# Kernel tuning notes

Measured on AMD Instinct MI355X. Metric: run time of the kernel, lower is better.

The kernel has to match this reference:

```python
import jax, jax.numpy as jnp
import numpy as np

B, T, D_IN = 4, 4096, 1024
H, DK, DV, D_MODEL = 16, 64, 64, 1024
EPS = 1e-6


def setup_inputs() -> dict:
    key = jax.random.key(0)
    ks = jax.random.split(key, 11)
    s_in = 1.0 / np.sqrt(D_IN)
    s_o = 1.0 / np.sqrt(H * DV)
    return {
        "query": jax.random.normal(ks[0], (B, T, D_IN), jnp.float32),
        "key": jax.random.normal(ks[1], (B, T, D_IN), jnp.float32),
        "value": jax.random.normal(ks[2], (B, T, D_IN), jnp.float32),
        "Wq": jax.random.normal(ks[3], (D_IN, H * DK), jnp.float32) * s_in,
        "bq": jnp.zeros((H * DK,), jnp.float32),
        "Wk": jax.random.normal(ks[4], (D_IN, H * DK), jnp.float32) * s_in,
        "bk": jnp.zeros((H * DK,), jnp.float32),
        "Wv": jax.random.normal(ks[5], (D_IN, H * DV), jnp.float32) * s_in,
        "bv": jnp.zeros((H * DV,), jnp.float32),
        "Wo": jax.random.normal(ks[6], (H * DV, D_MODEL), jnp.float32) * s_o,
        "bo": jnp.zeros((D_MODEL,), jnp.float32),
    }


def _phi(x):
    # ELU(x) + 1 feature map (positive kernel feature)
    return jax.nn.elu(x) + 1.0


def reference(query, key, value, Wq, bq, Wk, bk, Wv, bv, Wo, bo):
    b, t, _ = query.shape
    q = _phi(query @ Wq + bq).reshape(b, t, H, DK)   # [B,T,H,DK]
    k = _phi(key @ Wk + bk).reshape(b, t, H, DK)     # [B,T,H,DK]
    v = (value @ Wv + bv).reshape(b, t, H, DV)       # [B,T,H,DV]
    # KV accumulation over time: [B,H,DV,DK]
    kv = jnp.einsum('bthd,bthk->bhkd', k, v)
    # normalizer: q . sum_t(k)  -> [B,T,H]
    norm = 1.0 / (jnp.einsum('bthd,bhd->bth', q, k.sum(axis=1)) + EPS)
    attn = jnp.einsum('bthd,bhkd,bth->bthk', q, kv, norm)  # [B,T,H,DV]
    attn = attn.reshape(b, t, H * DV)
    return attn @ Wo + bo
```

## Files before the change

### kernel.cpp

```cpp
#include <hip/hip_runtime.h>

typedef __bf16 bf16;
typedef bf16 bf16x2 __attribute__((ext_vector_type(2)));
typedef bf16 bf16x8 __attribute__((ext_vector_type(8)));
typedef float f32x4 __attribute__((ext_vector_type(4)));

#define B_ 4
#define T_ 4096
#define H_ 16
#define DK_ 64
#define DV_ 64
#define DMODEL_ 1024
#define M_ (B_ * T_)
#define EPS_ 1e-6f

#define BARX()  asm volatile("s_barrier" ::: "memory")
#define LGKM0() asm volatile("s_waitcnt lgkmcnt(0)" ::: "memory")

__device__ __forceinline__ void async_ld16(const void* g, void* l) {
    __builtin_amdgcn_global_load_lds(
        (const __attribute__((address_space(1))) unsigned int*)g,
        (__attribute__((address_space(3))) unsigned int*)l,
        16, 0, 0);
}

struct TPtrs { const float* s[4]; bf16* d[4]; };

__global__ void transpose4(TPtrs p) {
    __shared__ bf16 t[32][33];
    const float* src = p.s[blockIdx.z];
    bf16*        dst = p.d[blockIdx.z];
    const int tx = threadIdx.x, ty = threadIdx.y;
    const int x  = blockIdx.x * 32 + tx;
    const int y0 = blockIdx.y * 32 + ty;
#pragma unroll
    for (int i = 0; i < 32; i += 8)
        t[ty + i][tx] = (bf16)src[(size_t)(y0 + i) * 1024 + x];
    __syncthreads();
    const int xo = blockIdx.y * 32 + tx;
    const int yo = blockIdx.x * 32 + ty;
#pragma unroll
    for (int i = 0; i < 32; i += 8)
        dst[(size_t)(yo + i) * 1024 + xo] = t[tx][ty + i];
}

__global__ __launch_bounds__(256) void cvt_kernel(
    const float* __restrict__ src, bf16* __restrict__ dst)
{
    const size_t i = (size_t)blockIdx.x * 256 + threadIdx.x;
    const float4* s = (const float4*)src + 2 * i;
    float4 a = s[0];
    float4 b = s[1];
    bf16x8 h;
    h[0] = (bf16)a.x; h[1] = (bf16)a.y; h[2] = (bf16)a.z; h[3] = (bf16)a.w;
    h[4] = (bf16)b.x; h[5] = (bf16)b.y; h[6] = (bf16)b.z; h[7] = (bf16)b.w;
    *(bf16x8*)(dst + 8 * i) = h;
}


__device__ __forceinline__ void stage_half(
    const bf16* __restrict__ G, int base_rc, int K,
    char* lds_op_buf, int t, int h, int w, int lane)
{
    const int r8   = lane >> 3;
    const int row  = h * 128 + w * 8 + r8;
    const int cole = (((lane & 7) ^ r8) << 3);
    const bf16* g = G + (size_t)(base_rc + row) * K + t * 64 + cole;
    char* l = lds_op_buf + h * 16384 + w * 1024;
    async_ld16(g, l);
    async_ld16(g + (size_t)64 * K, l + 8192);
}

template<int G>
__device__ __forceinline__ void read_a4(bf16x8 (&aF)[4][2], const char* ab,
                                        int arow, int fq, int l7) {
#pragma unroll
    for (int i = 0; i < 4; ++i)
#pragma unroll
        for (int ks = 0; ks < 2; ++ks)
            aF[i][ks] = *(const bf16x8*)(ab
                + (arow + (G * 4 + i) * 16) * 128
                + ((((ks << 2) + fq) ^ l7) << 4));
}

template<int JP>
__device__ __forceinline__ void read_b2(bf16x8 (&bF)[4][2], const char* bb,
                                        int brow, int fq, int l7) {
#pragma unroll
    for (int j = 0; j < 2; ++j)
#pragma unroll
        for (int ks = 0; ks < 2; ++ks)
            bF[JP * 2 + j][ks] = *(const bf16x8*)(bb
                + (brow + (JP * 2 + j) * 16) * 128
                + ((((ks << 2) + fq) ^ l7) << 4));
}

template<int G, int JP>
__device__ __forceinline__ void mfma_q(f32x4 (&acc)[8][4],
                                       const bf16x8 (&aF)[4][2],
                                       const bf16x8 (&bF)[4][2]) {
#pragma unroll
    for (int i = 0; i < 4; ++i)
#pragma unroll
        for (int j = 0; j < 2; ++j)
#pragma unroll
            for (int ks = 0; ks < 2; ++ks)
                acc[G * 4 + i][JP * 2 + j] =
                    __builtin_amdgcn_mfma_f32_16x16x32_bf16(
                        aF[i][ks], bF[JP * 2 + j][ks],
                        acc[G * 4 + i][JP * 2 + j], 0, 0, 0);
}

template<int ACT, int OUTMODE>
__global__ __launch_bounds__(512, 2) void gemm256_kernel(
    const bf16* __restrict__ A, const bf16* __restrict__ Bt,
    const float* __restrict__ bias, void* __restrict__ Cout,
    int M, int N, int K)
{
    __shared__ f32x4 smem4[8192];
    char* smem = (char*)smem4;
    char* Ab0 = smem;
    char* Ab1 = smem + 32768;
    char* Bb0 = smem + 65536;
    char* Bb1 = smem + 98304;

    const int tid  = threadIdx.x;
    const int w    = tid >> 6, lane = tid & 63;
    const int wrow = w >> 2,  wcol = w & 3;
    const int fr = lane & 15, fq = lane >> 4, l7 = lane & 7;
    const int arow = wrow * 128 + fr;
    const int brow = wcol * 64 + fr;

    const int nwg  = gridDim.x * gridDim.y;
    const int flat = blockIdx.y * gridDim.x + blockIdx.x;
    const int swz  = (flat & 7) * (nwg >> 3) + (flat >> 3);
    const int n0   = (swz % gridDim.x) * 256;
    const int m0   = (swz / gridDim.x) * 256;

    const int KT = K >> 6;

    f32x4  acc[8][4] = {};
    bf16x8 aF[4][2], bF[4][2];

    stage_half(Bt, n0, K, Bb0, 0, 0, w, lane);
    stage_half(Bt, n0, K, Bb0, 0, 1, w, lane);
    stage_half(A,  m0, K, Ab0, 0, 0, w, lane);
    stage_half(A,  m0, K, Ab0, 0, 1, w, lane);
    stage_half(Bt, n0, K, Bb1, 1, 0, w, lane);
    stage_half(Bt, n0, K, Bb1, 1, 1, w, lane);
    stage_half(A,  m0, K, Ab1, 1, 0, w, lane);
    stage_half(A,  m0, K, Ab1, 1, 1, w, lane);
    asm volatile("s_waitcnt vmcnt(8)" ::: "memory");
    BARX();

    for (int it = 0; it < (KT >> 1); ++it) {
        const int  t0   = it * 2, t1 = t0 + 1;
        const bool more = (it < (KT >> 1) - 1);

        read_a4<0>(aF, Ab0, arow, fq, l7);
        read_b2<0>(bF, Bb0, brow, fq, l7);
        asm volatile("s_waitcnt lgkmcnt(8)" ::: "memory");
        BARX(); LGKM0();
        __builtin_amdgcn_s_setprio(1);
        mfma_q<0, 0>(acc, aF, bF);
        __builtin_amdgcn_s_setprio(0);
        BARX();

        read_b2<1>(bF, Bb0, brow, fq, l7);
        BARX(); LGKM0();
        __builtin_amdgcn_s_setprio(1);
        mfma_q<0, 1>(acc, aF, bF);
        __builtin_amdgcn_s_setprio(0);
        BARX();

        read_a4<1>(aF, Ab0, arow, fq, l7);
        if (more) {
            stage_half(Bt, n0, K, Bb0, t0 + 2, 0, w, lane);
            stage_half(Bt, n0, K, Bb0, t0 + 2, 1, w, lane);
        }
        BARX(); LGKM0();
        __builtin_amdgcn_s_setprio(1);
        mfma_q<1, 0>(acc, aF, bF);
        __builtin_amdgcn_s_setprio(0);
        BARX();

        if (more) {
            stage_half(A, m0, K, Ab0, t0 + 2, 0, w, lane);
            stage_half(A, m0, K, Ab0, t0 + 2, 1, w, lane);
            asm volatile("s_waitcnt vmcnt(8)" ::: "memory");
        } else {
            asm volatile("s_waitcnt vmcnt(0)" ::: "memory");
        }
        BARX();
        __builtin_amdgcn_s_setprio(1);
        mfma_q<1, 1>(acc, aF, bF);
        __builtin_amdgcn_s_setprio(0);
        BARX();

        read_a4<0>(aF, Ab1, arow, fq, l7);
        read_b2<0>(bF, Bb1, brow, fq, l7);
        asm volatile("s_waitcnt lgkmcnt(8)" ::: "memory");
        BARX(); LGKM0();
        __builtin_amdgcn_s_setprio(1);
        mfma_q<0, 0>(acc, aF, bF);
        __builtin_amdgcn_s_setprio(0);
        BARX();

        read_b2<1>(bF, Bb1, brow, fq, l7);
        BARX(); LGKM0();
        __builtin_amdgcn_s_setprio(1);
        mfma_q<0, 1>(acc, aF, bF);
        __builtin_amdgcn_s_setprio(0);
        BARX();

        read_a4<1>(aF, Ab1, arow, fq, l7);
        if (more) {
            stage_half(Bt, n0, K, Bb1, t1 + 2, 0, w, lane);
            stage_half(Bt, n0, K, Bb1, t1 + 2, 1, w, lane);
        }
        BARX(); LGKM0();
        __builtin_amdgcn_s_setprio(1);
        mfma_q<1, 0>(acc, aF, bF);
        __builtin_amdgcn_s_setprio(0);
        BARX();

        if (more) {
            stage_half(A, m0, K, Ab1, t1 + 2, 0, w, lane);
            stage_half(A, m0, K, Ab1, t1 + 2, 1, w, lane);
            asm volatile("s_waitcnt vmcnt(8)" ::: "memory");
        }
        BARX();
        __builtin_amdgcn_s_setprio(1);
        mfma_q<1, 1>(acc, aF, bF);
        __builtin_amdgcn_s_setprio(0);
        BARX();
    }

    const size_t Ns = (size_t)N;
    if constexpr (OUTMODE == 2) {
        __syncthreads();
        char* eb = smem;
#pragma unroll
        for (int g = 0; g < 8; ++g)
#pragma unroll
            for (int j = 0; j < 4; ++j) {
                const int col = wcol * 64 + j * 16 + fr;
                const float bb = bias[n0 + col];
#pragma unroll
                for (int r = 0; r < 4; ++r) {
                    float x = acc[g][j][r] + bb;
                    if (ACT) x = (x > 0.0f) ? (x + 1.0f) : __expf(x);
                    const int row = wrow * 128 + g * 16 + fq * 4 + r;
                    *(bf16*)(eb + row * 512
                        + ((((col >> 3) ^ (row & 7)) << 4) | ((col & 7) << 1)))
                        = (bf16)x;
                }
            }
        __syncthreads();
        bf16* Cp = (bf16*)Cout;
#pragma unroll
        for (int o = 0; o < 16; ++o) {
            const int n = (tid >> 3) + (o & 3) * 64;
            const int m = (tid & 7) * 8 + (o >> 2) * 64;
            bf16x8 v;
#pragma unroll
            for (int e = 0; e < 8; ++e) {
                const int row = m + e;
                v[e] = *(const bf16*)(eb + row * 512
                        + ((((n >> 3) ^ (row & 7)) << 4) | ((n & 7) << 1)));
            }
            *(bf16x8*)(Cp + (size_t)(n0 + n) * M + m0 + m) = v;
        }
    } else {
#pragma unroll
        for (int g = 0; g < 8; ++g) {
#pragma unroll
            for (int j = 0; j < 4; ++j) {
                const int col = n0 + wcol * 64 + j * 16 + fr;
                const float bb = bias[col];
                const int row0 = m0 + wrow * 128 + g * 16 + fq * 4;
#pragma unroll
                for (int r = 0; r < 4; ++r) {
                    float x = acc[g][j][r] + bb;
                    if (ACT) x = (x > 0.0f) ? (x + 1.0f) : __expf(x);
                    if (OUTMODE == 1)
                        ((float*)Cout)[(size_t)(row0 + r) * Ns + col] = x;
                    else
                        ((bf16*)Cout)[(size_t)(row0 + r) * Ns + col] = (bf16)x;
                }
            }
        }
    }
}

__global__ __launch_bounds__(256) void kv_partial_kernel(
    const bf16* __restrict__ KT, const bf16* __restrict__ VT,
    float* __restrict__ kv_part, float* __restrict__ ksum_part)
{
    const int bh = blockIdx.y, b = bh >> 4, h = bh & 15;
    const int tc = blockIdx.x;
    __shared__ char lds[32768];

    const int tid = threadIdx.x, wv = tid >> 6, lane = tid & 63;
    const int fr = lane & 15, fq = lane >> 4, l7 = lane & 7;

    const int r1 = wv * 8 + (lane >> 3);
    const int c1 = ((lane & 7) ^ (r1 & 7)) << 3;
    const size_t g1 = (size_t)(h * 64 + r1) * M_ + (size_t)b * T_ + c1;
    const size_t g2 = g1 + (size_t)32 * M_;
    const int dstoff = (wv * 64 + lane) * 16;

    f32x4 acc[4] = {};
    float ksa = 0.0f;
    const int rk = tid >> 2, qk = tid & 3;

    {
        const size_t mo = (size_t)tc * 512;
        async_ld16(VT + g1 + mo, lds + dstoff);
        async_ld16(VT + g2 + mo, lds + 4096 + dstoff);
        async_ld16(KT + g1 + mo, lds + 8192 + dstoff);
        async_ld16(KT + g2 + mo, lds + 12288 + dstoff);
    }
    for (int it = 0; it < 8; ++it) {
        char* cur = lds + (it & 1) * 16384;
        char* nxt = lds + ((it & 1) ^ 1) * 16384;
        if (it < 7) {
            const size_t mo = (size_t)tc * 512 + (it + 1) * 64;
            async_ld16(VT + g1 + mo, nxt + dstoff);
            async_ld16(VT + g2 + mo, nxt + 4096 + dstoff);
            async_ld16(KT + g1 + mo, nxt + 8192 + dstoff);
            async_ld16(KT + g2 + mo, nxt + 12288 + dstoff);
            asm volatile("s_waitcnt vmcnt(4)" ::: "memory");
        } else {
            asm volatile("s_waitcnt vmcnt(0)" ::: "memory");
        }
        BARX();
        const char* Vb = cur;
        const char* Kb = cur + 8192;
#pragma unroll
        for (int ks = 0; ks < 2; ++ks) {
            bf16x8 av = *(const bf16x8*)(Vb + (wv * 16 + fr) * 128
                        + ((((ks << 2) + fq) ^ l7) << 4));
#pragma unroll
            for (int j = 0; j < 4; ++j) {
                bf16x8 bk = *(const bf16x8*)(Kb + (j * 16 + fr) * 128
                            + ((((ks << 2) + fq) ^ l7) << 4));
                acc[j] = __builtin_amdgcn_mfma_f32_16x16x32_bf16(
                    av, bk, acc[j], 0, 0, 0);
            }
        }
        {
            bf16x8 s0 = *(const bf16x8*)(Kb + rk * 128 + (((2 * qk) ^ (rk & 7)) << 4));
            bf16x8 s1 = *(const bf16x8*)(Kb + rk * 128 + (((2 * qk + 1) ^ (rk & 7)) << 4));
#pragma unroll
            for (int e = 0; e < 8; ++e) ksa += (float)s0[e] + (float)s1[e];
        }
        BARX();
    }

    float* kvp = kv_part + ((size_t)tc * 64 + bh) * 4096;
#pragma unroll
    for (int j = 0; j < 4; ++j)
#pragma unroll
        for (int r = 0; r < 4; ++r)
            kvp[(wv * 16 + fq * 4 + r) * 64 + j * 16 + fr] = acc[j][r];

    float s = ksa;
    s += __shfl_xor(s, 1);
    s += __shfl_xor(s, 2);
    if (qk == 0) ksum_part[((size_t)tc * 64 + bh) * 64 + rk] = s;
}

__global__ __launch_bounds__(256) void kv_reduce_kernel(
    const float* __restrict__ kv_part, const float* __restrict__ ksum_part,
    bf16* __restrict__ kvb, float* __restrict__ ksum)
{
    const int bh = blockIdx.x;
    const int tid = threadIdx.x;
    for (int e = tid; e < 4096; e += 256) {
        float s = 0.0f;
#pragma unroll
        for (int tc = 0; tc < 8; ++tc)
            s += kv_part[((size_t)tc * 64 + bh) * 4096 + e];
        kvb[(size_t)bh * 4096 + e] = (bf16)s;
    }
    if (tid < 64) {
        float s = 0.0f;
#pragma unroll
        for (int tc = 0; tc < 8; ++tc)
            s += ksum_part[((size_t)tc * 64 + bh) * 64 + tid];
        ksum[bh * 64 + tid] = s;
    }
}

__global__ __launch_bounds__(256) void attn_kernel(
    const bf16* __restrict__ Q, const bf16* __restrict__ kvb,
    const float* __restrict__ ksum, bf16* __restrict__ attn)
{
    const int bh = blockIdx.y;
    const int b  = bh >> 4;
    const int h  = bh & 15;
    const int t0 = blockIdx.x * 128;

    __shared__ bf16 As[128 * 64];
    __shared__ bf16 Bs[64 * 64];
    __shared__ float ksum_s[64];
    __shared__ float norm_s[128];

    const int tid  = threadIdx.x;
    const int wave = tid >> 6;
    const int lane = tid & 63;

    const bf16* Qbase = Q + ((size_t)(b * T_) + t0) * 1024 + h * 64;

#pragma unroll
    for (int r2 = 0; r2 < 4; ++r2) {
        const int c   = r2 * 256 + wave * 64 + lane;
        const int row = c >> 3;
        const int ko  = (c & 7) * 8;
        char* l = (char*)As + (size_t)(r2 * 256 + wave * 64) * 16;
        async_ld16(Qbase + (size_t)row * 1024 + ko, l);
    }
    {
        const float4* src = (const float4*)(kvb + (size_t)bh * 4096);
        float4* dst = (float4*)Bs;
        for (int e = tid; e < 512; e += 256) dst[e] = src[e];
    }
    if (tid < 64) ksum_s[tid] = ksum[bh * 64 + tid];
    __syncthreads();

    if (tid < 128) {
        float s = 0.0f;
#pragma unroll
        for (int u = 0; u < 8; ++u) {
            const int slot = (u + tid) & 7;
            bf16x8 v = *(const bf16x8*)&As[tid * 64 + slot * 8];
#pragma unroll
            for (int e = 0; e < 8; ++e) s += (float)v[e] * ksum_s[slot * 8 + e];
        }
        norm_s[tid] = 1.0f / (s + EPS_);
    }
    __syncthreads();

    const int fr  = lane & 15;
    const int fkq = lane >> 4;
    f32x4 acc[2][4] = {};
#pragma unroll
    for (int ks = 0; ks < 2; ++ks) {
        bf16x8 af[2], bfr[4];
#pragma unroll
        for (int i = 0; i < 2; ++i)
            af[i] = *(const bf16x8*)&As[(wave * 32 + i * 16 + fr) * 64 + ks * 32 + fkq * 8];
#pragma unroll
        for (int j = 0; j < 4; ++j)
            bfr[j] = *(const bf16x8*)&Bs[(j * 16 + fr) * 64 + ks * 32 + fkq * 8];
#pragma unroll
        for (int i = 0; i < 2; ++i)
#pragma unroll
            for (int j = 0; j < 4; ++j)
                acc[i][j] = __builtin_amdgcn_mfma_f32_16x16x32_bf16(
                    af[i], bfr[j], acc[i][j], 0, 0, 0);
    }

    bf16* out = attn + ((size_t)(b * T_) + t0) * 1024 + h * 64;
#pragma unroll
    for (int i = 0; i < 2; ++i)
#pragma unroll
        for (int j = 0; j < 4; ++j)
#pragma unroll
            for (int r = 0; r < 4; ++r) {
                const int row = wave * 32 + i * 16 + fkq * 4 + r;
                const int col = j * 16 + fr;
                out[(size_t)row * 1024 + col] = (bf16)(acc[i][j][r] * norm_s[row]);
            }
}

extern "C" void kernel_launch(void* const* d_in, const int* in_sizes, int n_in,
                              void* d_out, int out_size, void* d_ws, size_t ws_size,
                              hipStream_t stream) {
    const float* query = (const float*)d_in[0];
    const float* key_  = (const float*)d_in[1];
    const float* value = (const float*)d_in[2];
    const float* Wq = (const float*)d_in[3];
    const float* bq = (const float*)d_in[4];
    const float* Wk = (const float*)d_in[5];
    const float* bk = (const float*)d_in[6];
    const float* Wv = (const float*)d_in[7];
    const float* bv = (const float*)d_in[8];
    const float* Wo = (const float*)d_in[9];
    const float* bo = (const float*)d_in[10];

    char* ws = (char*)d_ws;
    char* out8 = (char*)d_out;
    const size_t MB = 1024 * 1024;
    bf16* WqT = (bf16*)(ws + 0 * MB);
    bf16* WkT = (bf16*)(ws + 2 * MB);
    bf16* WvT = (bf16*)(ws + 4 * MB);
    bf16* WoT = (bf16*)(ws + 6 * MB);
    bf16* CVT = (bf16*)(ws + 8 * MB);
    float* kv_part   = (float*)(ws + 40 * MB);
    float* ksum_part = (float*)(ws + 48 * MB);
    bf16*  kvb  = (bf16*)(ws + 48 * MB + 128 * 1024);
    float* ksum = (float*)(ws + 48 * MB + 640 * 1024);

    bf16* KTg  = (bf16*)out8;
    bf16* VTg  = (bf16*)(out8 + 32 * MB);
    bf16* Qb   = (bf16*)out8;
    bf16* ATTN = CVT;

    TPtrs tp;
    tp.s[0] = Wq;  tp.s[1] = Wk;  tp.s[2] = Wv;  tp.s[3] = Wo;
    tp.d[0] = WqT; tp.d[1] = WkT; tp.d[2] = WvT; tp.d[3] = WoT;
    transpose4<<<dim3(32, 32, 4), dim3(32, 8, 1), 0, stream>>>(tp);

    const int CVT_BLOCKS = M_ * 1024 / 8 / 256;
    const dim3 G256(4, 64);

    cvt_kernel<<<CVT_BLOCKS, 256, 0, stream>>>(key_, CVT);
    gemm256_kernel<1, 2><<<G256, 512, 0, stream>>>(CVT, WkT, bk, KTg, M_, 1024, 1024);

    cvt_kernel<<<CVT_BLOCKS, 256, 0, stream>>>(value, CVT);
    gemm256_kernel<0, 2><<<G256, 512, 0, stream>>>(CVT, WvT, bv, VTg, M_, 1024, 1024);

    kv_partial_kernel<<<dim3(8, 64), 256, 0, stream>>>(KTg, VTg, kv_part, ksum_part);
    kv_reduce_kernel<<<dim3(64), 256, 0, stream>>>(kv_part, ksum_part, kvb, ksum);

    cvt_kernel<<<CVT_BLOCKS, 256, 0, stream>>>(query, CVT);
    gemm256_kernel<1, 0><<<G256, 512, 0, stream>>>(CVT, WqT, bq, Qb, M_, 1024, 1024);

    attn_kernel<<<dim3(32, 64), 256, 0, stream>>>(Qb, kvb, ksum, ATTN);

    gemm256_kernel<0, 1><<<G256, 512, 0, stream>>>(ATTN, WoT, bo, (float*)d_out, M_, 1024, 1024);
}
```

Baseline: 425.2 us.

## Fuse attention application and normalizer into Q projection GEMM epilogue

Removes the separate attn_kernel by computing phi(Q) tiles in the Q GEMM epilogue and multiplying them in-register against a per-head KV matrix extended with ksum rows, stored as hi/lo bf16 split so the normalizer falls out of the same MFMA. This avoids writing and re-reading the full Q activation and drops one launch. It also rewrites the transposed-output epilogue (OUTMODE 2) so each thread does a single vectorized LDS read instead of gathering eight scalars. The costs are extra MFMA work per tile, more register pressure in the epilogue, and bf16 precision on the normalizer.

```diff
diff --git a/kernel.cpp b/kernel.cpp
--- a/kernel.cpp
+++ b/kernel.cpp
@@ -115,6 +115,7 @@
 __global__ __launch_bounds__(512, 2) void gemm256_kernel(
     const bf16* __restrict__ A, const bf16* __restrict__ Bt,
     const float* __restrict__ bias, void* __restrict__ Cout,
+    const bf16* __restrict__ KV2,
     int M, int N, int K)
 {
     __shared__ f32x4 smem4[8192];
@@ -244,15 +245,15 @@
         for (int g = 0; g < 8; ++g)
 #pragma unroll
             for (int j = 0; j < 4; ++j) {
-                const int col = wcol * 64 + j * 16 + fr;
-                const float bb = bias[n0 + col];
+                const int n = wcol * 64 + j * 16 + fr;
+                const float bb = bias[n0 + n];
 #pragma unroll
                 for (int r = 0; r < 4; ++r) {
                     float x = acc[g][j][r] + bb;
                     if (ACT) x = (x > 0.0f) ? (x + 1.0f) : __expf(x);
-                    const int row = wrow * 128 + g * 16 + fq * 4 + r;
-                    *(bf16*)(eb + row * 512
-                        + ((((col >> 3) ^ (row & 7)) << 4) | ((col & 7) << 1)))
+                    const int m = wrow * 128 + g * 16 + fq * 4 + r;
+                    *(bf16*)(eb + n * 512
+                        + ((((m >> 3) ^ (n & 7)) << 4) | ((m & 7) << 1)))
                         = (bf16)x;
                 }
             }
@@ -260,16 +261,69 @@
         bf16* Cp = (bf16*)Cout;
 #pragma unroll
         for (int o = 0; o < 16; ++o) {
-            const int n = (tid >> 3) + (o & 3) * 64;
-            const int m = (tid & 7) * 8 + (o >> 2) * 64;
-            bf16x8 v;
-#pragma unroll
-            for (int e = 0; e < 8; ++e) {
-                const int row = m + e;
-                v[e] = *(const bf16*)(eb + row * 512
-                        + ((((n >> 3) ^ (row & 7)) << 4) | ((n & 7) << 1)));
+            const int n    = (tid >> 5) + o * 16;
+            const int mblk = tid & 31;
+            bf16x8 v = *(const bf16x8*)(eb + n * 512
+                        + ((mblk ^ (n & 7)) << 4));
+            *(bf16x8*)(Cp + (size_t)(n0 + n) * M + m0 + mblk * 8) = v;
+        }
+    } else if constexpr (OUTMODE == 3) {
+        __syncthreads();
+        char* qb = smem + w * 16384;
+#pragma unroll
+        for (int g = 0; g < 8; ++g)
+#pragma unroll
+            for (int j = 0; j < 4; ++j) {
+                const int cq = j * 16 + fr;
+                const float bb = bias[n0 + wcol * 64 + cq];
+#pragma unroll
+                for (int r = 0; r < 4; ++r) {
+                    float x = acc[g][j][r] + bb;
+                    x = (x > 0.0f) ? (x + 1.0f) : __expf(x);
+                    const int row = g * 16 + fq * 4 + r;
+                    *(bf16*)(qb + row * 128
+                        + ((((cq >> 3) ^ (row & 7)) << 4) | ((cq & 7) << 1)))
+                        = (bf16)x;
+                }
             }
-            *(bf16x8*)(Cp + (size_t)(n0 + n) * M + m0 + m) = v;
+        __syncthreads();
+
+        const int hw = (n0 >> 6) + wcol;
+        const int bh = ((m0 >> 12) << 4) + hw;
+        const bf16* kvp2 = KV2 + (size_t)bh * 6144;
+        bf16x8 bO[6][2];
+#pragma unroll
+        for (int jj = 0; jj < 6; ++jj)
+#pragma unroll
+            for (int ks = 0; ks < 2; ++ks)
+                bO[jj][ks] = *(const bf16x8*)(kvp2
+                    + (jj * 16 + fr) * 64 + ks * 32 + fq * 8);
+
+        bf16* Cp = (bf16*)Cout;
+#pragma unroll
+        for (int g = 0; g < 8; ++g) {
+            bf16x8 aq[2];
+#pragma unroll
+            for (int ks = 0; ks < 2; ++ks)
+                aq[ks] = *(const bf16x8*)(qb + (g * 16 + fr) * 128
+                    + ((((ks << 2) + fq) ^ l7) << 4));
+            f32x4 o[6] = {};
+#pragma unroll
+            for (int ks = 0; ks < 2; ++ks)
+#pragma unroll
+                for (int jj = 0; jj < 6; ++jj)
+                    o[jj] = __builtin_amdgcn_mfma_f32_16x16x32_bf16(
+                        aq[ks], bO[jj][ks], o[jj], 0, 0, 0);
+#pragma unroll
+            for (int r = 0; r < 4; ++r) {
+                const float nrm = 1.0f / (o[4][r] + o[5][r] + EPS_);
+                const size_t row = (size_t)(m0 + wrow * 128 + g * 16
+                                            + fq * 4 + r);
+#pragma unroll
+                for (int jj = 0; jj < 4; ++jj)
+                    Cp[row * 1024 + n0 + wcol * 64 + jj * 16 + fr]
+                        = (bf16)(o[jj][r] * nrm);
+            }
         }
     } else {
 #pragma unroll
@@ -373,106 +427,31 @@
 
 __global__ __launch_bounds__(256) void kv_reduce_kernel(
     const float* __restrict__ kv_part, const float* __restrict__ ksum_part,
-    bf16* __restrict__ kvb, float* __restrict__ ksum)
+    bf16* __restrict__ kvb2)
 {
     const int bh = blockIdx.x;
     const int tid = threadIdx.x;
+    bf16* out = kvb2 + (size_t)bh * 6144;
     for (int e = tid; e < 4096; e += 256) {
         float s = 0.0f;
 #pragma unroll
         for (int tc = 0; tc < 8; ++tc)
             s += kv_part[((size_t)tc * 64 + bh) * 4096 + e];
-        kvb[(size_t)bh * 4096 + e] = (bf16)s;
+        out[e] = (bf16)s;
     }
     if (tid < 64) {
         float s = 0.0f;
 #pragma unroll
         for (int tc = 0; tc < 8; ++tc)
             s += ksum_part[((size_t)tc * 64 + bh) * 64 + tid];
-        ksum[bh * 64 + tid] = s;
+        const bf16 hi = (bf16)s;
+        const bf16 lo = (bf16)(s - (float)hi);
+#pragma unroll
+        for (int i = 0; i < 16; ++i) {
+            out[(64 + i) * 64 + tid] = hi;
+            out[(80 + i) * 64 + tid] = lo;
+        }
     }
-}
-
-__global__ __launch_bounds__(256) void attn_kernel(
-    const bf16* __restrict__ Q, const bf16* __restrict__ kvb,
-    const float* __restrict__ ksum, bf16* __restrict__ attn)
-{
-    const int bh = blockIdx.y;
-    const int b  = bh >> 4;
-    const int h  = bh & 15;
-    const int t0 = blockIdx.x * 128;
-
-    __shared__ bf16 As[128 * 64];
-    __shared__ bf16 Bs[64 * 64];
-    __shared__ float ksum_s[64];
-    __shared__ float norm_s[128];
-
-    const int tid  = threadIdx.x;
-    const int wave = tid >> 6;
-    const int lane = tid & 63;
-
-    const bf16* Qbase = Q + ((size_t)(b * T_) + t0) * 1024 + h * 64;
-
-#pragma unroll
-    for (int r2 = 0; r2 < 4; ++r2) {
-        const int c   = r2 * 256 + wave * 64 + lane;
-        const int row = c >> 3;
-        const int ko  = (c & 7) * 8;
-        char* l = (char*)As + (size_t)(r2 * 256 + wave * 64) * 16;
-        async_ld16(Qbase + (size_t)row * 1024 + ko, l);
-    }
-    {
-        const float4* src = (const float4*)(kvb + (size_t)bh * 4096);
-        float4* dst = (float4*)Bs;
-        for (int e = tid; e < 512; e += 256) dst[e] = src[e];
-    }
-    if (tid < 64) ksum_s[tid] = ksum[bh * 64 + tid];
-    __syncthreads();
-
-    if (tid < 128) {
-        float s = 0.0f;
-#pragma unroll
-        for (int u = 0; u < 8; ++u) {
-            const int slot = (u + tid) & 7;
-            bf16x8 v = *(const bf16x8*)&As[tid * 64 + slot * 8];
-#pragma unroll
-            for (int e = 0; e < 8; ++e) s += (float)v[e] * ksum_s[slot * 8 + e];
-        }
-        norm_s[tid] = 1.0f / (s + EPS_);
-    }
-    __syncthreads();
-
-    const int fr  = lane & 15;
-    const int fkq = lane >> 4;
-    f32x4 acc[2][4] = {};
-#pragma unroll
-    for (int ks = 0; ks < 2; ++ks) {
-        bf16x8 af[2], bfr[4];
-#pragma unroll
-        for (int i = 0; i < 2; ++i)
-            af[i] = *(const bf16x8*)&As[(wave * 32 + i * 16 + fr) * 64 + ks * 32 + fkq * 8];
-#pragma unroll
-        for (int j = 0; j < 4; ++j)
-            bfr[j] = *(const bf16x8*)&Bs[(j * 16 + fr) * 64 + ks * 32 + fkq * 8];
-#pragma unroll
-        for (int i = 0; i < 2; ++i)
-#pragma unroll
-            for (int j = 0; j < 4; ++j)
-                acc[i][j] = __builtin_amdgcn_mfma_f32_16x16x32_bf16(
-                    af[i], bfr[j], acc[i][j], 0, 0, 0);
-    }
-
-    bf16* out = attn + ((size_t)(b * T_) + t0) * 1024 + h * 64;
-#pragma unroll
-    for (int i = 0; i < 2; ++i)
-#pragma unroll
-        for (int j = 0; j < 4; ++j)
-#pragma unroll
-            for (int r = 0; r < 4; ++r) {
-                const int row = wave * 32 + i * 16 + fkq * 4 + r;
-                const int col = j * 16 + fr;
-                out[(size_t)row * 1024 + col] = (bf16)(acc[i][j][r] * norm_s[row]);
-            }
 }
 
 extern "C" void kernel_launch(void* const* d_in, const int* in_sizes, int n_in,
@@ -500,12 +479,11 @@
     bf16* CVT = (bf16*)(ws + 8 * MB);
     float* kv_part   = (float*)(ws + 40 * MB);
     float* ksum_part = (float*)(ws + 48 * MB);
-    bf16*  kvb  = (bf16*)(ws + 48 * MB + 128 * 1024);
-    float* ksum = (float*)(ws + 48 * MB + 640 * 1024);
 
     bf16* KTg  = (bf16*)out8;
     bf16* VTg  = (bf16*)(out8 + 32 * MB);
-    bf16* Qb   = (bf16*)out8;
+    bf16* Qcvt = (bf16*)out8;
+    bf16* kvb2 = (bf16*)(out8 + 32 * MB);
     bf16* ATTN = CVT;
 
     TPtrs tp;
@@ -517,18 +495,16 @@
     const dim3 G256(4, 64);
 
     cvt_kernel<<<CVT_BLOCKS, 256, 0, stream>>>(key_, CVT);
-    gemm256_kernel<1, 2><<<G256, 512, 0, stream>>>(CVT, WkT, bk, KTg, M_, 1024, 1024);
+    gemm256_kernel<1, 2><<<G256, 512, 0, stream>>>(CVT, WkT, bk, KTg, nullptr, M_, 1024, 1024);
 
     cvt_kernel<<<CVT_BLOCKS, 256, 0, stream>>>(value, CVT);
-    gemm256_kernel<0, 2><<<G256, 512, 0, stream>>>(CVT, WvT, bv, VTg, M_, 1024, 1024);
+    gemm256_kernel<0, 2><<<G256, 512, 0, stream>>>(CVT, WvT, bv, VTg, nullptr, M_, 1024, 1024);
 
     kv_partial_kernel<<<dim3(8, 64), 256, 0, stream>>>(KTg, VTg, kv_part, ksum_part);
-    kv_reduce_kernel<<<dim3(64), 256, 0, stream>>>(kv_part, ksum_part, kvb, ksum);
-
-    cvt_kernel<<<CVT_BLOCKS, 256, 0, stream>>>(query, CVT);
-    gemm256_kernel<1, 0><<<G256, 512, 0, stream>>>(CVT, WqT, bq, Qb, M_, 1024, 1024);
-
-    attn_kernel<<<dim3(32, 64), 256, 0, stream>>>(Qb, kvb, ksum, ATTN);
-
-    gemm256_kernel<0, 1><<<G256, 512, 0, stream>>>(ATTN, WoT, bo, (float*)d_out, M_, 1024, 1024);
-}
+    kv_reduce_kernel<<<dim3(64), 256, 0, stream>>>(kv_part, ksum_part, kvb2);
+
+    cvt_kernel<<<CVT_BLOCKS, 256, 0, stream>>>(query, Qcvt);
+    gemm256_kernel<1, 3><<<G256, 512, 0, stream>>>(Qcvt, WqT, bq, ATTN, kvb2, M_, 1024, 1024);
+
+    gemm256_kernel<0, 1><<<G256, 512, 0, stream>>>(ATTN, WoT, bo, (float*)d_out, nullptr, M_, 1024, 1024);
+}
```

Result: faster. 404.6 us (-4.9%).
